# Kernel optimization log

Measured on AMD Instinct MI355X. Metric: run time of the kernel, lower is better.

Reference implementation:

```python
import jax, jax.numpy as jnp
import numpy as np


def setup_inputs() -> dict:
    key = jax.random.key(0)
    k1, k2, k3, k4 = jax.random.split(key, 4)
    B, K, M, X, Y = 64, 4, 3, 256, 256
    predictions = jax.random.uniform(k1, (B, K, X, Y), dtype=jnp.float32)
    inputs = jax.random.normal(k2, (B, M, X, Y), dtype=jnp.float32)
    heart = jax.random.randint(k3, (B, 1, X, Y), 0, 2, dtype=jnp.int32)
    mu_data = jax.random.normal(k4, (K, M), dtype=jnp.float32)
    return {"predictions": predictions, "inputs": inputs, "heart": heart, "mu_data": mu_data}


def reference(predictions, inputs, heart, mu_data):
    eps = 1e-10
    # Boolean-mask gather is equivalent to multiplying by the 0/1 mask, since
    # everything downstream is a sum over the masked positions.
    mask = (heart[:, 0] == 1).astype(predictions.dtype)          # [B, X, Y]
    pm = predictions * mask[:, None]                             # [B, K, X, Y]
    num = jnp.einsum('bkxy,bmxy->bkm', pm, inputs)               # weighted sums
    den = jnp.sum(pm, axis=(2, 3)) + eps                         # [B, K]
    mu_mean = jnp.mean(num / den[..., None], axis=0)             # [K, M]
    return jnp.sum((mu_data - mu_mean) ** 2)
```

## Files before the change

### kernel.cpp

```cpp
#include <hip/hip_runtime.h>

#define B_      64
#define K_      4
#define M_      3
#define NPIX    65536
#define CHUNKS  32
#define TPB     256
#define ITERS   2
#define NV      16

__global__ __launch_bounds__(TPB) void partial_kernel(
    const float* __restrict__ pred,
    const float* __restrict__ inp,
    const int*   __restrict__ heart,
    float* __restrict__ partial_ws)
{
    const int c = blockIdx.x;
    const int b = blockIdx.y;
    const int base = c * (NPIX / CHUNKS) + (int)threadIdx.x * (4 * ITERS);

    float val[NV];
#pragma unroll
    for (int i = 0; i < NV; ++i) val[i] = 0.0f;

#pragma unroll
    for (int it = 0; it < ITERS; ++it) {
        const int pix = base + it * 4;

        const int4 h = *reinterpret_cast<const int4*>(heart + (size_t)b * NPIX + pix);
        float4 mask;
        mask.x = (h.x == 1) ? 1.0f : 0.0f;
        mask.y = (h.y == 1) ? 1.0f : 0.0f;
        mask.z = (h.z == 1) ? 1.0f : 0.0f;
        mask.w = (h.w == 1) ? 1.0f : 0.0f;

        float4 in[M_];
#pragma unroll
        for (int m = 0; m < M_; ++m)
            in[m] = *reinterpret_cast<const float4*>(inp + ((size_t)b * M_ + m) * NPIX + pix);

#pragma unroll
        for (int k = 0; k < K_; ++k) {
            float4 p = *reinterpret_cast<const float4*>(pred + ((size_t)b * K_ + k) * NPIX + pix);
            float4 pm;
            pm.x = p.x * mask.x; pm.y = p.y * mask.y;
            pm.z = p.z * mask.z; pm.w = p.w * mask.w;
            val[k] += (pm.x + pm.y) + (pm.z + pm.w);
#pragma unroll
            for (int m = 0; m < M_; ++m)
                val[4 + k * M_ + m] += pm.x * in[m].x + pm.y * in[m].y
                                     + pm.z * in[m].z + pm.w * in[m].w;
        }
    }

#pragma unroll
    for (int off = 32; off > 0; off >>= 1) {
#pragma unroll
        for (int i = 0; i < NV; ++i)
            val[i] += __shfl_down(val[i], off, 64);
    }

    __shared__ float smem[TPB / 64][NV];
    const int lane = threadIdx.x & 63;
    const int wave = threadIdx.x >> 6;
    if (lane == 0) {
#pragma unroll
        for (int i = 0; i < NV; ++i) smem[wave][i] = val[i];
    }
    __syncthreads();

    if (threadIdx.x < NV) {
        const float s = smem[0][threadIdx.x] + smem[1][threadIdx.x]
                      + smem[2][threadIdx.x] + smem[3][threadIdx.x];
        partial_ws[((size_t)b * CHUNKS + c) * NV + threadIdx.x] = s;
    }
}

__global__ __launch_bounds__(64) void finalize_kernel(
    const float* __restrict__ partial_ws,
    const float* __restrict__ mu_data,
    float* __restrict__ out)
{
    const int b = threadIdx.x;
    float acc[NV];
#pragma unroll
    for (int i = 0; i < NV; ++i) acc[i] = 0.0f;
    for (int c = 0; c < CHUNKS; ++c) {
        const float* p = partial_ws + ((size_t)b * CHUNKS + c) * NV;
#pragma unroll
        for (int i = 0; i < NV; ++i) acc[i] += p[i];
    }

    float r[K_ * M_];
#pragma unroll
    for (int k = 0; k < K_; ++k) {
        const float inv = 1.0f / (acc[k] + 1e-10f);
#pragma unroll
        for (int m = 0; m < M_; ++m)
            r[k * M_ + m] = acc[4 + k * M_ + m] * inv;
    }
#pragma unroll
    for (int off = 32; off > 0; off >>= 1) {
#pragma unroll
        for (int i = 0; i < K_ * M_; ++i)
            r[i] += __shfl_down(r[i], off, 64);
    }
    if (b == 0) {
        float s = 0.0f;
#pragma unroll
        for (int i = 0; i < K_ * M_; ++i) {
            const float d = mu_data[i] - r[i] * (1.0f / (float)B_);
            s += d * d;
        }
        out[0] = s;
    }
}

extern "C" void kernel_launch(void* const* d_in, const int* in_sizes, int n_in,
                              void* d_out, int out_size, void* d_ws, size_t ws_size,
                              hipStream_t stream) {
    const float* pred    = (const float*)d_in[0];
    const float* inp     = (const float*)d_in[1];
    const int*   heart   = (const int*)d_in[2];
    const float* mu_data = (const float*)d_in[3];
    float* out = (float*)d_out;

    float* partial_ws = (float*)d_ws;

    dim3 grid(CHUNKS, B_);
    partial_kernel<<<grid, TPB, 0, stream>>>(pred, inp, heart, partial_ws);
    finalize_kernel<<<1, 64, 0, stream>>>(partial_ws, mu_data, out);
}
```

Measured before the change: 155.4 us.

## Double-buffer loads with coalesced strided pixel loop and fewer chunks

Cuts the chunks per batch from 32 to 8, so each thread now handles 8 float4 groups instead of 2. Accesses move to a block-wide stride so each wave's loads stay contiguous, and a two-batch software pipeline issues the next batch's loads before consuming the current one. The goal is to keep more memory requests in flight per thread and to cut per-block reduction and partial-writing overhead. In exchange register pressure rises and the grid shrinks to 512 blocks, which may leave less parallelism to hide latency.

```diff
diff --git a/kernel.cpp b/kernel.cpp
--- a/kernel.cpp
+++ b/kernel.cpp
@@ -4,10 +4,54 @@
 #define K_      4
 #define M_      3
 #define NPIX    65536
-#define CHUNKS  32
+#define CHUNKS  8
 #define TPB     256
-#define ITERS   2
+#define IT      8
+#define SPAN    (NPIX / CHUNKS)
+#define STRIDE  (TPB * 4)
 #define NV      16
+
+struct LoadBatch {
+    int4   h;
+    float4 in[M_];
+    float4 p[K_];
+};
+
+__device__ __forceinline__ void issue_loads(
+    LoadBatch& L,
+    const float* __restrict__ pred_b,
+    const float* __restrict__ inp_b,
+    const int*   __restrict__ heart_b,
+    int pix)
+{
+    L.h = *reinterpret_cast<const int4*>(heart_b + pix);
+#pragma unroll
+    for (int m = 0; m < M_; ++m)
+        L.in[m] = *reinterpret_cast<const float4*>(inp_b + (size_t)m * NPIX + pix);
+#pragma unroll
+    for (int k = 0; k < K_; ++k)
+        L.p[k] = *reinterpret_cast<const float4*>(pred_b + (size_t)k * NPIX + pix);
+}
+
+__device__ __forceinline__ void consume(const LoadBatch& L, float* val)
+{
+    float4 mask;
+    mask.x = (L.h.x == 1) ? 1.0f : 0.0f;
+    mask.y = (L.h.y == 1) ? 1.0f : 0.0f;
+    mask.z = (L.h.z == 1) ? 1.0f : 0.0f;
+    mask.w = (L.h.w == 1) ? 1.0f : 0.0f;
+#pragma unroll
+    for (int k = 0; k < K_; ++k) {
+        float4 pm;
+        pm.x = L.p[k].x * mask.x; pm.y = L.p[k].y * mask.y;
+        pm.z = L.p[k].z * mask.z; pm.w = L.p[k].w * mask.w;
+        val[k] += (pm.x + pm.y) + (pm.z + pm.w);
+#pragma unroll
+        for (int m = 0; m < M_; ++m)
+            val[4 + k * M_ + m] += pm.x * L.in[m].x + pm.y * L.in[m].y
+                                 + pm.z * L.in[m].z + pm.w * L.in[m].w;
+    }
+}
 
 __global__ __launch_bounds__(TPB) void partial_kernel(
     const float* __restrict__ pred,
@@ -17,40 +61,24 @@
 {
     const int c = blockIdx.x;
     const int b = blockIdx.y;
-    const int base = c * (NPIX / CHUNKS) + (int)threadIdx.x * (4 * ITERS);
+    const int base = c * SPAN + (int)threadIdx.x * 4;
+
+    const float* pred_b  = pred  + (size_t)b * K_ * NPIX;
+    const float* inp_b   = inp   + (size_t)b * M_ * NPIX;
+    const int*   heart_b = heart + (size_t)b * NPIX;
 
     float val[NV];
 #pragma unroll
     for (int i = 0; i < NV; ++i) val[i] = 0.0f;
 
+    LoadBatch A, Bb;
+    issue_loads(A, pred_b, inp_b, heart_b, base);
 #pragma unroll
-    for (int it = 0; it < ITERS; ++it) {
-        const int pix = base + it * 4;
-
-        const int4 h = *reinterpret_cast<const int4*>(heart + (size_t)b * NPIX + pix);
-        float4 mask;
-        mask.x = (h.x == 1) ? 1.0f : 0.0f;
-        mask.y = (h.y == 1) ? 1.0f : 0.0f;
-        mask.z = (h.z == 1) ? 1.0f : 0.0f;
-        mask.w = (h.w == 1) ? 1.0f : 0.0f;
-
-        float4 in[M_];
-#pragma unroll
-        for (int m = 0; m < M_; ++m)
-            in[m] = *reinterpret_cast<const float4*>(inp + ((size_t)b * M_ + m) * NPIX + pix);
-
-#pragma unroll
-        for (int k = 0; k < K_; ++k) {
-            float4 p = *reinterpret_cast<const float4*>(pred + ((size_t)b * K_ + k) * NPIX + pix);
-            float4 pm;
-            pm.x = p.x * mask.x; pm.y = p.y * mask.y;
-            pm.z = p.z * mask.z; pm.w = p.w * mask.w;
-            val[k] += (pm.x + pm.y) + (pm.z + pm.w);
-#pragma unroll
-            for (int m = 0; m < M_; ++m)
-                val[4 + k * M_ + m] += pm.x * in[m].x + pm.y * in[m].y
-                                     + pm.z * in[m].z + pm.w * in[m].w;
-        }
+    for (int j = 0; j < IT; j += 2) {
+        if (j + 1 < IT) issue_loads(Bb, pred_b, inp_b, heart_b, base + (j + 1) * STRIDE);
+        consume(A, val);
+        if (j + 2 < IT) issue_loads(A, pred_b, inp_b, heart_b, base + (j + 2) * STRIDE);
+        consume(Bb, val);
     }
 
 #pragma unroll
```

After: 153.4 us. Within noise of the previous version (-1.3%).

## Double-buffer tiles through LDS with async global_load_lds and fewer chunks

Applied to the files above, without the earlier changes.

Replaces direct per-thread vector global loads with a double-buffered pipeline. Each wave issues async global-to-LDS copies (`__builtin_amdgcn_global_load_lds`) for the next 1024-pixel tile of heart, inputs and predictions while the current tile is consumed from LDS. Chunks per batch drop from 32 to 8, so each block loops over 8 stages. The aim is to keep more memory requests in flight and overlap loads with compute. In exchange each block uses 64KB of LDS, the grid is 4x smaller, and correctness relies on the barrier waiting for the async copies to finish.

```diff
diff --git a/kernel.cpp b/kernel.cpp
--- a/kernel.cpp
+++ b/kernel.cpp
@@ -4,10 +4,36 @@
 #define K_      4
 #define M_      3
 #define NPIX    65536
-#define CHUNKS  32
+#define CHUNKS  8
 #define TPB     256
-#define ITERS   2
+#define SPAN    (NPIX / CHUNKS)
+#define TILE    1024
+#define STAGES  (SPAN / TILE)
 #define NV      16
+
+typedef __attribute__((address_space(1))) const void gas_t;
+typedef __attribute__((address_space(3))) void las_t;
+__device__ __forceinline__ void gload16(const void* g, void* l) {
+    __builtin_amdgcn_global_load_lds((gas_t*)g, (las_t*)l, 16, 0, 0);
+}
+
+__device__ __forceinline__ void load_stage(
+    const float* __restrict__ pred_b, const float* __restrict__ inp_b,
+    const int* __restrict__ heart_b, float* buf, int tile_px, int wv, int ln)
+{
+#pragma unroll
+    for (int j = 0; j < 2; ++j) {
+        const int sid = 2 * wv + j;
+        const float* g;
+        if (sid == 0)      g = (const float*)(heart_b + tile_px);
+        else if (sid <= 3) g = inp_b  + (size_t)(sid - 1) * NPIX + tile_px;
+        else               g = pred_b + (size_t)(sid - 4) * NPIX + tile_px;
+        float* l = buf + sid * TILE;
+#pragma unroll
+        for (int i = 0; i < 4; ++i)
+            gload16(g + i * 256 + ln * 4, l + i * 256);
+    }
+}
 
 __global__ __launch_bounds__(TPB) void partial_kernel(
     const float* __restrict__ pred,
@@ -17,17 +43,32 @@
 {
     const int c = blockIdx.x;
     const int b = blockIdx.y;
-    const int base = c * (NPIX / CHUNKS) + (int)threadIdx.x * (4 * ITERS);
+    const int wv = threadIdx.x >> 6;
+    const int ln = threadIdx.x & 63;
+    const int t  = threadIdx.x;
+
+    const float* pred_b  = pred  + (size_t)b * K_ * NPIX;
+    const float* inp_b   = inp   + (size_t)b * M_ * NPIX;
+    const int*   heart_b = heart + (size_t)b * NPIX;
+    const int base_px = c * SPAN;
+
+    __shared__ float lds[2][8 * TILE];
+    __shared__ float smem[TPB / 64][NV];
 
     float val[NV];
 #pragma unroll
     for (int i = 0; i < NV; ++i) val[i] = 0.0f;
 
-#pragma unroll
-    for (int it = 0; it < ITERS; ++it) {
-        const int pix = base + it * 4;
+    load_stage(pred_b, inp_b, heart_b, lds[0], base_px, wv, ln);
 
-        const int4 h = *reinterpret_cast<const int4*>(heart + (size_t)b * NPIX + pix);
+    for (int s = 0; s < STAGES; ++s) {
+        __syncthreads();
+        if (s + 1 < STAGES)
+            load_stage(pred_b, inp_b, heart_b, lds[(s + 1) & 1],
+                       base_px + (s + 1) * TILE, wv, ln);
+
+        const float* buf = lds[s & 1];
+        const int4 h = reinterpret_cast<const int4*>(buf)[t];
         float4 mask;
         mask.x = (h.x == 1) ? 1.0f : 0.0f;
         mask.y = (h.y == 1) ? 1.0f : 0.0f;
@@ -37,11 +78,11 @@
         float4 in[M_];
 #pragma unroll
         for (int m = 0; m < M_; ++m)
-            in[m] = *reinterpret_cast<const float4*>(inp + ((size_t)b * M_ + m) * NPIX + pix);
+            in[m] = reinterpret_cast<const float4*>(buf + (1 + m) * TILE)[t];
 
 #pragma unroll
         for (int k = 0; k < K_; ++k) {
-            float4 p = *reinterpret_cast<const float4*>(pred + ((size_t)b * K_ + k) * NPIX + pix);
+            const float4 p = reinterpret_cast<const float4*>(buf + (4 + k) * TILE)[t];
             float4 pm;
             pm.x = p.x * mask.x; pm.y = p.y * mask.y;
             pm.z = p.z * mask.z; pm.w = p.w * mask.w;
@@ -60,19 +101,15 @@
             val[i] += __shfl_down(val[i], off, 64);
     }
 
-    __shared__ float smem[TPB / 64][NV];
-    const int lane = threadIdx.x & 63;
-    const int wave = threadIdx.x >> 6;
-    if (lane == 0) {
+    if (ln == 0) {
 #pragma unroll
-        for (int i = 0; i < NV; ++i) smem[wave][i] = val[i];
+        for (int i = 0; i < NV; ++i) smem[wv][i] = val[i];
     }
     __syncthreads();
 
-    if (threadIdx.x < NV) {
-        const float s = smem[0][threadIdx.x] + smem[1][threadIdx.x]
-                      + smem[2][threadIdx.x] + smem[3][threadIdx.x];
-        partial_ws[((size_t)b * CHUNKS + c) * NV + threadIdx.x] = s;
+    if (t < NV) {
+        const float s = smem[0][t] + smem[1][t] + smem[2][t] + smem[3][t];
+        partial_ws[((size_t)b * CHUNKS + c) * NV + t] = s;
     }
 }
 
```

After: 155.4 us. About the same (-0.0%).
